# Performance work log

Hardware: AMD Instinct MI355X
Metric: run time of the kernel (lower is better)

Reference implementation:

```python
import jax, jax.numpy as jnp
import numpy as np

B, N, C = 2, 2048, 1024
H = 16
D = C // H  # head dim = 64


def setup_inputs() -> dict:
    key = jax.random.key(0)
    ks = jax.random.split(key, 11)
    s = 1.0 / np.sqrt(C)
    inp = {
        "q": jax.random.normal(ks[0], (B, N, C), jnp.float32),
        "k": jax.random.normal(ks[1], (B, N, C), jnp.float32),
        "v": jax.random.normal(ks[2], (B, N, C), jnp.float32),
        # Linear params (kernel shape [in, out], as in flax)
        "Wq": jax.random.normal(ks[3], (C, C), jnp.float32) * s,
        "bq": jnp.zeros((C,), jnp.float32),
        "Wk": jax.random.normal(ks[4], (C, C), jnp.float32) * s,
        "bk": jnp.zeros((C,), jnp.float32),
        "Wv": jax.random.normal(ks[5], (C, C), jnp.float32) * s,
        "bv": jnp.zeros((C,), jnp.float32),
        "Wo": jax.random.normal(ks[6], (C, C), jnp.float32) * s,
        "bo": jnp.zeros((C,), jnp.float32),
    }
    return inp


def reference(q, k, v, Wq, bq, Wk, bk, Wv, bv, Wo, bo):
    # QKV projections: (B,N,C) @ (C,C) + bias
    qh = (q @ Wq + bq).reshape(B, N, H, D).transpose(0, 2, 1, 3)  # b h n d
    kh = (k @ Wk + bk).reshape(B, N, H, D).transpose(0, 2, 1, 3)
    vh = (v @ Wv + bv).reshape(B, N, H, D).transpose(0, 2, 1, 3)
    scale = 1.0 / np.sqrt(D)
    attn = jnp.einsum('bhqd,bhkd->bhqk', qh * scale, kh)  # full NxN scores
    attn = jax.nn.softmax(attn, axis=-1)
    out = jnp.einsum('bhqk,bhkd->bhqd', attn, vh)
    out = out.transpose(0, 2, 1, 3).reshape(B, N, C)
    return out @ Wo + bo
```

## Files before the change

kernel.cpp:

```cpp
#include <hip/hip_runtime.h>
#include <hip/hip_bf16.h>
#include <math.h>


typedef __attribute__((ext_vector_type(8))) short bf16x8;
typedef __attribute__((ext_vector_type(4))) short bf16x4;
typedef __attribute__((ext_vector_type(4))) float f32x4;
typedef __attribute__((ext_vector_type(2))) unsigned int u32x2;

__device__ __forceinline__ short f2bf(float f) {
    union { float f; unsigned u; } x; x.f = f;
    unsigned r = x.u + 0x7fffu + ((x.u >> 16) & 1u);
    return (short)(r >> 16);
}

__device__ __forceinline__ unsigned cvt_pk_bf16(float lo, float hi) {
    unsigned r;
    asm volatile("v_cvt_pk_bf16_f32 %0, %1, %2" : "=v"(r) : "v"(lo), "v"(hi));
    return r;
}

__global__ __launch_bounds__(256) void prep_w(const float* __restrict__ Wq,
                                              const float* __restrict__ Wk,
                                              const float* __restrict__ Wv,
                                              const float* __restrict__ Wo,
                                              short* __restrict__ wt) {
    __shared__ float tile[32][33];
    const float* W = blockIdx.z == 0 ? Wq : blockIdx.z == 1 ? Wk
                   : blockIdx.z == 2 ? Wv : Wo;
    short* dst = wt + (size_t)blockIdx.z * 1048576;
    const int bx = blockIdx.x * 32, by = blockIdx.y * 32;
    const int tx = threadIdx.x & 31, ty = threadIdx.x >> 5;
#pragma unroll
    for (int i = 0; i < 32; i += 8)
        tile[ty + i][tx] = W[(size_t)(by + ty + i) * 1024 + bx + tx];
    __syncthreads();
#pragma unroll
    for (int i = 0; i < 32; i += 8)
        dst[(size_t)(bx + ty + i) * 1024 + by + tx] = f2bf(tile[tx][ty + i]);
}

__global__ __launch_bounds__(256) void gemm_qkv(const float* __restrict__ qA,
                                                const float* __restrict__ kA,
                                                const float* __restrict__ vA,
                                                const short* __restrict__ wt,
                                                const float* __restrict__ bq,
                                                const float* __restrict__ bk,
                                                const float* __restrict__ bv,
                                                short* __restrict__ qh,
                                                short* __restrict__ khp,
                                                short* __restrict__ vtp,
                                                float qscale) {
    __shared__ short As[128 * 32];
    __shared__ short Bs[64 * 32];
    const int tid = threadIdx.x;
    const int l = tid & 63, w = tid >> 6;
    const int wr = w >> 1, wc = w & 1;
    const int row16 = l & 15, lg = l >> 4;
    const int m0 = blockIdx.x * 128;
    const int n0 = blockIdx.y * 64;
    const int z = blockIdx.z;

    const float* A = z == 0 ? qA : z == 1 ? kA : vA;
    const short* Wt = wt + (size_t)z * 1048576;
    const float* bias = z == 0 ? bq : z == 1 ? bk : bv;
    const float scale = z == 0 ? qscale : 1.0f;
    short* outp = z == 0 ? qh : z == 1 ? khp : vtp;

    const int ar = tid >> 1, ac = (tid & 1) * 16;
    const int br = tid >> 2, bc = (tid & 3) * 8;

    f32x4 acc[4][2] = {};

    f32x4 x0, x1, x2, x3; bf16x8 bfrag;
    {
        const float* src = A + (size_t)(m0 + ar) * 1024 + ac;
        x0 = ((const f32x4*)src)[0]; x1 = ((const f32x4*)src)[1];
        x2 = ((const f32x4*)src)[2]; x3 = ((const f32x4*)src)[3];
        bfrag = *(const bf16x8*)(Wt + (size_t)(n0 + br) * 1024 + bc);
    }

    for (int t = 0; t < 32; ++t) {
        __syncthreads();
        bf16x8 sa0, sa1;
#pragma unroll
        for (int j = 0; j < 4; ++j) {
            sa0[j] = f2bf(x0[j]); sa0[4 + j] = f2bf(x1[j]);
            sa1[j] = f2bf(x2[j]); sa1[4 + j] = f2bf(x3[j]);
        }
        *(bf16x8*)&As[ar * 32 + ac]     = sa0;
        *(bf16x8*)&As[ar * 32 + ac + 8] = sa1;
        *(bf16x8*)&Bs[br * 32 + bc]     = bfrag;
        __syncthreads();
        if (t < 31) {
            const int k0 = (t + 1) * 32;
            const float* src = A + (size_t)(m0 + ar) * 1024 + k0 + ac;
            x0 = ((const f32x4*)src)[0]; x1 = ((const f32x4*)src)[1];
            x2 = ((const f32x4*)src)[2]; x3 = ((const f32x4*)src)[3];
            bfrag = *(const bf16x8*)(Wt + (size_t)(n0 + br) * 1024 + k0 + bc);
        }
        bf16x8 af[4], bf2[2];
#pragma unroll
        for (int m = 0; m < 4; ++m)
            af[m] = *(const bf16x8*)&As[(wr * 64 + m * 16 + row16) * 32 + lg * 8];
#pragma unroll
        for (int n = 0; n < 2; ++n)
            bf2[n] = *(const bf16x8*)&Bs[(wc * 32 + n * 16 + row16) * 32 + lg * 8];
#pragma unroll
        for (int m = 0; m < 4; ++m)
#pragma unroll
            for (int n = 0; n < 2; ++n)
                acc[m][n] = __builtin_amdgcn_mfma_f32_16x16x32_bf16(af[m], bf2[n], acc[m][n], 0, 0, 0);
    }

#pragma unroll
    for (int n = 0; n < 2; ++n) {
        const int col = n0 + wc * 32 + n * 16 + row16;
        const float bvl = bias[col];
        const int h = col >> 6, d = col & 63;
#pragma unroll
        for (int m = 0; m < 4; ++m) {
#pragma unroll
            for (int r = 0; r < 4; ++r) {
                const int row = m0 + wr * 64 + m * 16 + lg * 4 + r;
                const float val = (acc[m][n][r] + bvl) * scale;
                const int b = row >> 11, nt = row & 2047;
                if (z != 2)
                    outp[(((size_t)(b * 16 + h)) * 2048 + nt) * 64 + d] = f2bf(val);
                else
                    outp[(((size_t)(b * 16 + h)) * 64 + d) * 2048 + nt] = f2bf(val);
            }
        }
    }
}

__global__ __launch_bounds__(256) void gemm_out(const short* __restrict__ Ab,
                                                const short* __restrict__ Wt,
                                                const float* __restrict__ bias,
                                                float* __restrict__ outp) {
    __shared__ short As[128 * 32];
    __shared__ short Bs[64 * 32];
    const int tid = threadIdx.x;
    const int l = tid & 63, w = tid >> 6;
    const int wr = w >> 1, wc = w & 1;
    const int row16 = l & 15, lg = l >> 4;
    const int m0 = blockIdx.x * 128;
    const int n0 = blockIdx.y * 64;

    const int ar = tid >> 1, ac = (tid & 1) * 16;
    const int br = tid >> 2, bc = (tid & 3) * 8;

    f32x4 acc[4][2] = {};

    bf16x8 sa0, sa1, bfrag;
    sa0 = *(const bf16x8*)(Ab + (size_t)(m0 + ar) * 1024 + ac);
    sa1 = *(const bf16x8*)(Ab + (size_t)(m0 + ar) * 1024 + ac + 8);
    bfrag = *(const bf16x8*)(Wt + (size_t)(n0 + br) * 1024 + bc);

    for (int t = 0; t < 32; ++t) {
        __syncthreads();
        *(bf16x8*)&As[ar * 32 + ac]     = sa0;
        *(bf16x8*)&As[ar * 32 + ac + 8] = sa1;
        *(bf16x8*)&Bs[br * 32 + bc]     = bfrag;
        __syncthreads();
        if (t < 31) {
            const int k0 = (t + 1) * 32;
            sa0 = *(const bf16x8*)(Ab + (size_t)(m0 + ar) * 1024 + k0 + ac);
            sa1 = *(const bf16x8*)(Ab + (size_t)(m0 + ar) * 1024 + k0 + ac + 8);
            bfrag = *(const bf16x8*)(Wt + (size_t)(n0 + br) * 1024 + k0 + bc);
        }
        bf16x8 af[4], bf2[2];
#pragma unroll
        for (int m = 0; m < 4; ++m)
            af[m] = *(const bf16x8*)&As[(wr * 64 + m * 16 + row16) * 32 + lg * 8];
#pragma unroll
        for (int n = 0; n < 2; ++n)
            bf2[n] = *(const bf16x8*)&Bs[(wc * 32 + n * 16 + row16) * 32 + lg * 8];
#pragma unroll
        for (int m = 0; m < 4; ++m)
#pragma unroll
            for (int n = 0; n < 2; ++n)
                acc[m][n] = __builtin_amdgcn_mfma_f32_16x16x32_bf16(af[m], bf2[n], acc[m][n], 0, 0, 0);
    }

#pragma unroll
    for (int n = 0; n < 2; ++n) {
        const int col = n0 + wc * 32 + n * 16 + row16;
        const float bvl = bias[col];
#pragma unroll
        for (int m = 0; m < 4; ++m) {
#pragma unroll
            for (int r = 0; r < 4; ++r) {
                const int row = m0 + wr * 64 + m * 16 + lg * 4 + r;
                outp[(size_t)row * 1024 + col] = acc[m][n][r] + bvl;
            }
        }
    }
}

__device__ __forceinline__ void attn_step(int t,
                                          const short* __restrict__ kbase,
                                          const short* __restrict__ vbase,
                                          bf16x8 (&kc)[4][2], bf16x8 (&kn)[4][2],
                                          bf16x8 (&qf)[2][2], f32x4 (&oac)[2][4],
                                          float (&lsum)[2],
                                          short* prow0, short* prow1,
                                          int row16, int lg) {
    const int kvn = t * 64;
    const int kvnn = ((t + 1) & 31) * 64;

    f32x4 s[2][4] = {};
#pragma unroll
    for (int kt = 0; kt < 4; ++kt)
#pragma unroll
        for (int kk = 0; kk < 2; ++kk) {
            s[0][kt] = __builtin_amdgcn_mfma_f32_16x16x32_bf16(kc[kt][kk], qf[0][kk], s[0][kt], 0, 0, 0);
            s[1][kt] = __builtin_amdgcn_mfma_f32_16x16x32_bf16(kc[kt][kk], qf[1][kk], s[1][kt], 0, 0, 0);
        }

    bf16x8 vf[4][2];
#pragma unroll
    for (int dt = 0; dt < 4; ++dt)
#pragma unroll
        for (int kk = 0; kk < 2; ++kk)
            vf[dt][kk] = *(const bf16x8*)&vbase[(size_t)(dt * 16 + row16) * 2048 + kvn + kk * 32 + lg * 8];
#pragma unroll
    for (int kt = 0; kt < 4; ++kt)
#pragma unroll
        for (int kk = 0; kk < 2; ++kk)
            kn[kt][kk] = *(const bf16x8*)&kbase[(size_t)(kvnn + kt * 16 + row16) * 64 + kk * 32 + lg * 8];

#pragma unroll
    for (int qt = 0; qt < 2; ++qt)
#pragma unroll
        for (int kt = 0; kt < 4; ++kt)
#pragma unroll
            for (int r = 0; r < 4; ++r) {
                const float p = exp2f(s[qt][kt][r]);
                s[qt][kt][r] = p;
                lsum[qt] += p;
            }

    short* prow[2] = {prow0, prow1};
#pragma unroll
    for (int qt = 0; qt < 2; ++qt)
#pragma unroll
        for (int kt = 0; kt < 4; ++kt) {
            u32x2 pk;
            pk.x = cvt_pk_bf16(s[qt][kt][0], s[qt][kt][1]);
            pk.y = cvt_pk_bf16(s[qt][kt][2], s[qt][kt][3]);
            *(u32x2*)&prow[qt][kt * 16 + lg * 4] = pk;
        }
    asm volatile("s_waitcnt lgkmcnt(0)" ::: "memory");
    bf16x8 pf[2][2];
#pragma unroll
    for (int qt = 0; qt < 2; ++qt)
#pragma unroll
        for (int kk = 0; kk < 2; ++kk)
            pf[qt][kk] = *(const bf16x8*)&prow[qt][kk * 32 + lg * 8];
    asm volatile("" ::: "memory");

#pragma unroll
    for (int dt = 0; dt < 4; ++dt)
#pragma unroll
        for (int kk = 0; kk < 2; ++kk) {
            oac[0][dt] = __builtin_amdgcn_mfma_f32_16x16x32_bf16(pf[0][kk], vf[dt][kk], oac[0][dt], 0, 0, 0);
            oac[1][dt] = __builtin_amdgcn_mfma_f32_16x16x32_bf16(pf[1][kk], vf[dt][kk], oac[1][dt], 0, 0, 0);
        }
}

__global__ __launch_bounds__(256) void attn_kernel(const short* __restrict__ qh,
                                                   const short* __restrict__ kh,
                                                   const short* __restrict__ vt,
                                                   short* __restrict__ aout) {
    __shared__ short Pls[8][16 * 72];

    const int tid = threadIdx.x;
    const int l = tid & 63, w = tid >> 6;
    const int row16 = l & 15, lg = l >> 4;
    const int bh = blockIdx.y;
    const int q0 = blockIdx.x * 128 + w * 32;

    const short* kbase = kh + (size_t)bh * 2048 * 64;
    const short* vbase = vt + (size_t)bh * 64 * 2048;

    bf16x8 qf[2][2];
#pragma unroll
    for (int qt = 0; qt < 2; ++qt)
#pragma unroll
        for (int kk = 0; kk < 2; ++kk)
            qf[qt][kk] = *(const bf16x8*)&qh[((size_t)bh * 2048 + q0 + qt * 16 + row16) * 64 + kk * 32 + lg * 8];

    f32x4 oac[2][4] = {};
    float lsum[2] = {0.f, 0.f};

    short* prow0 = &Pls[w * 2 + 0][row16 * 72];
    short* prow1 = &Pls[w * 2 + 1][row16 * 72];

    bf16x8 kfA[4][2], kfB[4][2];
#pragma unroll
    for (int kt = 0; kt < 4; ++kt)
#pragma unroll
        for (int kk = 0; kk < 2; ++kk)
            kfA[kt][kk] = *(const bf16x8*)&kbase[(size_t)(kt * 16 + row16) * 64 + kk * 32 + lg * 8];

    for (int tt = 0; tt < 32; tt += 2) {
        attn_step(tt,     kbase, vbase, kfA, kfB, qf, oac, lsum, prow0, prow1, row16, lg);
        attn_step(tt + 1, kbase, vbase, kfB, kfA, qf, oac, lsum, prow0, prow1, row16, lg);
    }

#pragma unroll
    for (int qt = 0; qt < 2; ++qt) {
        lsum[qt] += __shfl_xor(lsum[qt], 16, 64);
        lsum[qt] += __shfl_xor(lsum[qt], 32, 64);
    }
    const int b = bh >> 4, h = bh & 15;
    const float inv0 = 1.f / lsum[0], inv1 = 1.f / lsum[1];
#pragma unroll
    for (int qt = 0; qt < 2; ++qt) {
#pragma unroll
        for (int r = 0; r < 4; ++r) {
            const float iv = __shfl(qt == 0 ? inv0 : inv1, lg * 4 + r, 64);
            const int qrow = q0 + qt * 16 + lg * 4 + r;
#pragma unroll
            for (int dt = 0; dt < 4; ++dt) {
                const int c = h * 64 + dt * 16 + row16;
                aout[((size_t)b * 2048 + qrow) * 1024 + c] = f2bf(oac[qt][dt][r] * iv);
            }
        }
    }
}

extern "C" void kernel_launch(void* const* d_in, const int* in_sizes, int n_in,
                              void* d_out, int out_size, void* d_ws, size_t ws_size,
                              hipStream_t stream) {
    const float* q  = (const float*)d_in[0];
    const float* k  = (const float*)d_in[1];
    const float* v  = (const float*)d_in[2];
    const float* Wq = (const float*)d_in[3];
    const float* bq = (const float*)d_in[4];
    const float* Wk = (const float*)d_in[5];
    const float* bk = (const float*)d_in[6];
    const float* Wv = (const float*)d_in[7];
    const float* bv = (const float*)d_in[8];
    const float* Wo = (const float*)d_in[9];
    const float* bo = (const float*)d_in[10];

    char* ws = (char*)d_ws;
    short* wt   = (short*)ws;
    short* qh   = (short*)(ws + (8u  << 20));
    short* khp  = (short*)(ws + (16u << 20));
    short* vt   = (short*)(ws + (24u << 20));
    short* aout = (short*)(ws + (32u << 20));

    const float qscale = 0.125f * 1.44269504088896340736f;

    prep_w<<<dim3(32, 32, 4), 256, 0, stream>>>(Wq, Wk, Wv, Wo, wt);
    gemm_qkv<<<dim3(32, 16, 3), 256, 0, stream>>>(q, k, v, wt, bq, bk, bv,
                                                  qh, khp, vt, qscale);
    attn_kernel<<<dim3(16, 32), 256, 0, stream>>>(qh, khp, vt, aout);
    gemm_out<<<dim3(32, 16), 256, 0, stream>>>(aout, wt + 3145728, bo, (float*)d_out);
}
```

Before: 221.5 us.

## Software-pipeline attention loop and compute softmax row sums via MFMA with ones

Restructures the attention inner loop so the PV product of tile t-1 overlaps with the QK scores and exp of tile t. The P fragments read back from LDS and the V fragments are carried across iterations, and the V loads are issued after the PV MFMAs. The scalar exp-sum accumulation plus cross-lane shuffles are replaced by an extra MFMA of P against a ones vector, which also puts each row sum in the lane layout the output normalisation needs. This adds MFMA work and sums the bf16-rounded probabilities instead of the fp32 ones, which slightly changes the normaliser.

```diff
diff --git a/kernel.cpp b/kernel.cpp
--- a/kernel.cpp
+++ b/kernel.cpp
@@ -198,77 +198,6 @@
     }
 }
 
-__device__ __forceinline__ void attn_step(int t,
-                                          const short* __restrict__ kbase,
-                                          const short* __restrict__ vbase,
-                                          bf16x8 (&kc)[4][2], bf16x8 (&kn)[4][2],
-                                          bf16x8 (&qf)[2][2], f32x4 (&oac)[2][4],
-                                          float (&lsum)[2],
-                                          short* prow0, short* prow1,
-                                          int row16, int lg) {
-    const int kvn = t * 64;
-    const int kvnn = ((t + 1) & 31) * 64;
-
-    f32x4 s[2][4] = {};
-#pragma unroll
-    for (int kt = 0; kt < 4; ++kt)
-#pragma unroll
-        for (int kk = 0; kk < 2; ++kk) {
-            s[0][kt] = __builtin_amdgcn_mfma_f32_16x16x32_bf16(kc[kt][kk], qf[0][kk], s[0][kt], 0, 0, 0);
-            s[1][kt] = __builtin_amdgcn_mfma_f32_16x16x32_bf16(kc[kt][kk], qf[1][kk], s[1][kt], 0, 0, 0);
-        }
-
-    bf16x8 vf[4][2];
-#pragma unroll
-    for (int dt = 0; dt < 4; ++dt)
-#pragma unroll
-        for (int kk = 0; kk < 2; ++kk)
-            vf[dt][kk] = *(const bf16x8*)&vbase[(size_t)(dt * 16 + row16) * 2048 + kvn + kk * 32 + lg * 8];
-#pragma unroll
-    for (int kt = 0; kt < 4; ++kt)
-#pragma unroll
-        for (int kk = 0; kk < 2; ++kk)
-            kn[kt][kk] = *(const bf16x8*)&kbase[(size_t)(kvnn + kt * 16 + row16) * 64 + kk * 32 + lg * 8];
-
-#pragma unroll
-    for (int qt = 0; qt < 2; ++qt)
-#pragma unroll
-        for (int kt = 0; kt < 4; ++kt)
-#pragma unroll
-            for (int r = 0; r < 4; ++r) {
-                const float p = exp2f(s[qt][kt][r]);
-                s[qt][kt][r] = p;
-                lsum[qt] += p;
-            }
-
-    short* prow[2] = {prow0, prow1};
-#pragma unroll
-    for (int qt = 0; qt < 2; ++qt)
-#pragma unroll
-        for (int kt = 0; kt < 4; ++kt) {
-            u32x2 pk;
-            pk.x = cvt_pk_bf16(s[qt][kt][0], s[qt][kt][1]);
-            pk.y = cvt_pk_bf16(s[qt][kt][2], s[qt][kt][3]);
-            *(u32x2*)&prow[qt][kt * 16 + lg * 4] = pk;
-        }
-    asm volatile("s_waitcnt lgkmcnt(0)" ::: "memory");
-    bf16x8 pf[2][2];
-#pragma unroll
-    for (int qt = 0; qt < 2; ++qt)
-#pragma unroll
-        for (int kk = 0; kk < 2; ++kk)
-            pf[qt][kk] = *(const bf16x8*)&prow[qt][kk * 32 + lg * 8];
-    asm volatile("" ::: "memory");
-
-#pragma unroll
-    for (int dt = 0; dt < 4; ++dt)
-#pragma unroll
-        for (int kk = 0; kk < 2; ++kk) {
-            oac[0][dt] = __builtin_amdgcn_mfma_f32_16x16x32_bf16(pf[0][kk], vf[dt][kk], oac[0][dt], 0, 0, 0);
-            oac[1][dt] = __builtin_amdgcn_mfma_f32_16x16x32_bf16(pf[1][kk], vf[dt][kk], oac[1][dt], 0, 0, 0);
-        }
-}
-
 __global__ __launch_bounds__(256) void attn_kernel(const short* __restrict__ qh,
                                                    const short* __restrict__ kh,
                                                    const short* __restrict__ vt,
@@ -291,36 +220,133 @@
         for (int kk = 0; kk < 2; ++kk)
             qf[qt][kk] = *(const bf16x8*)&qh[((size_t)bh * 2048 + q0 + qt * 16 + row16) * 64 + kk * 32 + lg * 8];
 
+    bf16x8 ones;
+#pragma unroll
+    for (int j = 0; j < 8; ++j) ones[j] = (short)0x3F80;
+
     f32x4 oac[2][4] = {};
-    float lsum[2] = {0.f, 0.f};
+    f32x4 lacc[2] = {};
 
     short* prow0 = &Pls[w * 2 + 0][row16 * 72];
     short* prow1 = &Pls[w * 2 + 1][row16 * 72];
-
-    bf16x8 kfA[4][2], kfB[4][2];
+    short* prow[2] = {prow0, prow1};
+
+    bf16x8 kf[4][2], vf[4][2], pf[2][2];
 #pragma unroll
     for (int kt = 0; kt < 4; ++kt)
 #pragma unroll
+        for (int kk = 0; kk < 2; ++kk) {
+            kf[kt][kk] = *(const bf16x8*)&kbase[(size_t)(kt * 16 + row16) * 64 + kk * 32 + lg * 8];
+            vf[kt][kk] = *(const bf16x8*)&vbase[(size_t)(kt * 16 + row16) * 2048 + kk * 32 + lg * 8];
+        }
+
+    {
+        f32x4 s[2][4] = {};
+#pragma unroll
+        for (int kt = 0; kt < 4; ++kt)
+#pragma unroll
+            for (int kk = 0; kk < 2; ++kk) {
+                s[0][kt] = __builtin_amdgcn_mfma_f32_16x16x32_bf16(kf[kt][kk], qf[0][kk], s[0][kt], 0, 0, 0);
+                s[1][kt] = __builtin_amdgcn_mfma_f32_16x16x32_bf16(kf[kt][kk], qf[1][kk], s[1][kt], 0, 0, 0);
+            }
+#pragma unroll
+        for (int kt = 0; kt < 4; ++kt)
+#pragma unroll
+            for (int kk = 0; kk < 2; ++kk)
+                kf[kt][kk] = *(const bf16x8*)&kbase[(size_t)(64 + kt * 16 + row16) * 64 + kk * 32 + lg * 8];
+#pragma unroll
+        for (int qt = 0; qt < 2; ++qt)
+#pragma unroll
+            for (int kt = 0; kt < 4; ++kt) {
+                u32x2 pk;
+                pk.x = cvt_pk_bf16(exp2f(s[qt][kt][0]), exp2f(s[qt][kt][1]));
+                pk.y = cvt_pk_bf16(exp2f(s[qt][kt][2]), exp2f(s[qt][kt][3]));
+                *(u32x2*)&prow[qt][kt * 16 + lg * 4] = pk;
+            }
+        asm volatile("s_waitcnt lgkmcnt(0)" ::: "memory");
+#pragma unroll
+        for (int qt = 0; qt < 2; ++qt)
+#pragma unroll
+            for (int kk = 0; kk < 2; ++kk)
+                pf[qt][kk] = *(const bf16x8*)&prow[qt][kk * 32 + lg * 8];
+        asm volatile("" ::: "memory");
+    }
+
+    for (int t = 1; t < 32; ++t) {
+        const int kvn = t * 64;
+        const int kvnn = ((t + 1) & 31) * 64;
+
+        f32x4 s[2][4] = {};
+#pragma unroll
+        for (int kt = 0; kt < 4; ++kt)
+#pragma unroll
+            for (int kk = 0; kk < 2; ++kk) {
+                s[0][kt] = __builtin_amdgcn_mfma_f32_16x16x32_bf16(kf[kt][kk], qf[0][kk], s[0][kt], 0, 0, 0);
+                s[1][kt] = __builtin_amdgcn_mfma_f32_16x16x32_bf16(kf[kt][kk], qf[1][kk], s[1][kt], 0, 0, 0);
+            }
+#pragma unroll
+        for (int kt = 0; kt < 4; ++kt)
+#pragma unroll
+            for (int kk = 0; kk < 2; ++kk)
+                kf[kt][kk] = *(const bf16x8*)&kbase[(size_t)(kvnn + kt * 16 + row16) * 64 + kk * 32 + lg * 8];
+
+#pragma unroll
+        for (int qt = 0; qt < 2; ++qt)
+#pragma unroll
+            for (int kt = 0; kt < 4; ++kt) {
+                u32x2 pk;
+                pk.x = cvt_pk_bf16(exp2f(s[qt][kt][0]), exp2f(s[qt][kt][1]));
+                pk.y = cvt_pk_bf16(exp2f(s[qt][kt][2]), exp2f(s[qt][kt][3]));
+                *(u32x2*)&prow[qt][kt * 16 + lg * 4] = pk;
+            }
+
+#pragma unroll
+        for (int dt = 0; dt < 4; ++dt)
+#pragma unroll
+            for (int kk = 0; kk < 2; ++kk) {
+                oac[0][dt] = __builtin_amdgcn_mfma_f32_16x16x32_bf16(pf[0][kk], vf[dt][kk], oac[0][dt], 0, 0, 0);
+                oac[1][dt] = __builtin_amdgcn_mfma_f32_16x16x32_bf16(pf[1][kk], vf[dt][kk], oac[1][dt], 0, 0, 0);
+            }
+#pragma unroll
+        for (int qt = 0; qt < 2; ++qt)
+#pragma unroll
+            for (int kk = 0; kk < 2; ++kk)
+                lacc[qt] = __builtin_amdgcn_mfma_f32_16x16x32_bf16(pf[qt][kk], ones, lacc[qt], 0, 0, 0);
+
+#pragma unroll
+        for (int dt = 0; dt < 4; ++dt)
+#pragma unroll
+            for (int kk = 0; kk < 2; ++kk)
+                vf[dt][kk] = *(const bf16x8*)&vbase[(size_t)(dt * 16 + row16) * 2048 + kvn + kk * 32 + lg * 8];
+
+        asm volatile("s_waitcnt lgkmcnt(0)" ::: "memory");
+#pragma unroll
+        for (int qt = 0; qt < 2; ++qt)
+#pragma unroll
+            for (int kk = 0; kk < 2; ++kk)
+                pf[qt][kk] = *(const bf16x8*)&prow[qt][kk * 32 + lg * 8];
+        asm volatile("" ::: "memory");
+    }
+
+#pragma unroll
+    for (int dt = 0; dt < 4; ++dt)
+#pragma unroll
+        for (int kk = 0; kk < 2; ++kk) {
+            oac[0][dt] = __builtin_amdgcn_mfma_f32_16x16x32_bf16(pf[0][kk], vf[dt][kk], oac[0][dt], 0, 0, 0);
+            oac[1][dt] = __builtin_amdgcn_mfma_f32_16x16x32_bf16(pf[1][kk], vf[dt][kk], oac[1][dt], 0, 0, 0);
+        }
+#pragma unroll
+    for (int qt = 0; qt < 2; ++qt)
+#pragma unroll
         for (int kk = 0; kk < 2; ++kk)
-            kfA[kt][kk] = *(const bf16x8*)&kbase[(size_t)(kt * 16 + row16) * 64 + kk * 32 + lg * 8];
-
-    for (int tt = 0; tt < 32; tt += 2) {
-        attn_step(tt,     kbase, vbase, kfA, kfB, qf, oac, lsum, prow0, prow1, row16, lg);
-        attn_step(tt + 1, kbase, vbase, kfB, kfA, qf, oac, lsum, prow0, prow1, row16, lg);
-    }
-
+            lacc[qt] = __builtin_amdgcn_mfma_f32_16x16x32_bf16(pf[qt][kk], ones, lacc[qt], 0, 0, 0);
+
+    const int b = bh >> 4, h = bh & 15;
 #pragma unroll
     for (int qt = 0; qt < 2; ++qt) {
-        lsum[qt] += __shfl_xor(lsum[qt], 16, 64);
-        lsum[qt] += __shfl_xor(lsum[qt], 32, 64);
-    }
-    const int b = bh >> 4, h = bh & 15;
-    const float inv0 = 1.f / lsum[0], inv1 = 1.f / lsum[1];
-#pragma unroll
-    for (int qt = 0; qt < 2; ++qt) {
 #pragma unroll
         for (int r = 0; r < 4; ++r) {
-            const float iv = __shfl(qt == 0 ? inv0 : inv1, lg * 4 + r, 64);
+            const float iv = 1.f / lacc[qt][r];
             const int qrow = q0 + qt * 16 + lg * 4 + r;
 #pragma unroll
             for (int dt = 0; dt < 4; ++dt) {
```

New measurement: 221.0 us. No clear change (-0.2%).
